# Kernel tuning notes

Measured on AMD Instinct MI355X. Metric: run time of the kernel, lower is better.

## Reference

```python
import jax, jax.numpy as jnp
import numpy as np

N_NODES = 20000
N_EDGES = 320000
NUM_FEAT = 14
DIM = 256


def setup_inputs() -> dict:
    key = jax.random.key(0)
    ks = jax.random.split(key, 12)
    x = jax.random.normal(ks[0], (N_NODES, NUM_FEAT), dtype=jnp.float32)
    edge_index = jax.random.randint(ks[1], (2, N_EDGES), 0, N_NODES, dtype=jnp.int64)
    edge_weight = jax.random.uniform(ks[2], (N_EDGES,), dtype=jnp.float32)

    def lin_w(k, fan_in, fan_out):
        b = 1.0 / np.sqrt(fan_in)
        return jax.random.uniform(k, (fan_in, fan_out), jnp.float32, -b, b)

    params = {
        'W1_rel': lin_w(ks[3], NUM_FEAT, DIM), 'b1_rel': jnp.zeros((DIM,), jnp.float32),
        'W1_root': lin_w(ks[4], NUM_FEAT, DIM),
        'W2_rel': lin_w(ks[5], DIM, DIM), 'b2_rel': jnp.zeros((DIM,), jnp.float32),
        'W2_root': lin_w(ks[6], DIM, DIM),
        'W3_rel': lin_w(ks[7], DIM, DIM), 'b3_rel': jnp.zeros((DIM,), jnp.float32),
        'W3_root': lin_w(ks[8], DIM, DIM),
        'W_lin': lin_w(ks[9], 3 * DIM, DIM), 'b_lin': jnp.zeros((DIM,), jnp.float32),
    }
    return {'x': x, 'edge_index': edge_index, 'edge_weight': edge_weight, **params}


def _graph_conv(x, src, dst, ew, W_rel, b_rel, W_root, n_nodes):
    # message: x_j * w_ij ; aggr='mean' over incoming edges (count, not weight sum)
    msg = x[src] * ew[:, None]                               # [E, F]
    agg = jax.ops.segment_sum(msg, dst, num_segments=n_nodes)  # [N, F]
    cnt = jax.ops.segment_sum(jnp.ones_like(ew), dst, num_segments=n_nodes)
    mean = agg / jnp.maximum(cnt, 1.0)[:, None]
    return mean @ W_rel + b_rel + x @ W_root


def reference(x, edge_index, edge_weight,
              W1_rel, b1_rel, W1_root,
              W2_rel, b2_rel, W2_root,
              W3_rel, b3_rel, W3_root,
              W_lin, b_lin):
    src, dst = edge_index[0], edge_index[1]
    n = x.shape[0]
    # eval mode: dropout is identity
    x1 = jax.nn.relu(_graph_conv(x, src, dst, edge_weight, W1_rel, b1_rel, W1_root, n))
    x2 = jax.nn.relu(_graph_conv(x1, src, dst, edge_weight, W2_rel, b2_rel, W2_root, n))
    x3 = jax.nn.relu(_graph_conv(x2, src, dst, edge_weight, W3_rel, b3_rel, W3_root, n))
    xc = jnp.concatenate([x1, x2, x3], axis=-1)              # [N, 3*DIM]
    return xc @ W_lin + b_lin
```

## Files before the change

### kernel.cpp

```cpp
#include <hip/hip_runtime.h>

#define N_NODES 20000
#define N_EDGES 320000
#define NFEAT 14
#define DIM 256

typedef short bf16x8 __attribute__((ext_vector_type(8)));
typedef float f32x4 __attribute__((ext_vector_type(4)));

__device__ __forceinline__ float b2f(unsigned short u) {
    union { unsigned int u; float f; } v; v.u = ((unsigned int)u) << 16; return v.f;
}
__device__ __forceinline__ unsigned short f2b(float f) {
    union { float f; unsigned int u; } v; v.f = f;
    unsigned int r = v.u + 0x7fffu + ((v.u >> 16) & 1u);
    return (unsigned short)(r >> 16);
}


__global__ __launch_bounds__(256) void k_degree(const int* __restrict__ ei, int* __restrict__ cnt) {
    int e = blockIdx.x * 256 + threadIdx.x;
    if (e < N_EDGES) atomicAdd(&cnt[ei[N_EDGES + e]], 1);
}

__global__ __launch_bounds__(256) void k_alloc(const int* __restrict__ cnt,
                                               int* __restrict__ total,
                                               int* __restrict__ row_ptr,
                                               int* __restrict__ cursor) {
    int i = blockIdx.x * 256 + threadIdx.x;
    int lane = threadIdx.x & 63;
    int deg = (i < N_NODES) ? cnt[i] : 0;
    int s = deg;
    for (int o = 1; o < 64; o <<= 1) { int t = __shfl_up(s, o); if (lane >= o) s += t; }
    int wsum = __shfl(s, 63);
    int base = 0;
    if (lane == 63) base = atomicAdd(total, wsum);
    base = __shfl(base, 63);
    int excl = base + s - deg;
    if (i < N_NODES) { row_ptr[i] = excl; cursor[i] = excl; }
}

__global__ __launch_bounds__(256) void k_fill(const int* __restrict__ ei, const float* __restrict__ ew,
                                              int* __restrict__ cursor,
                                              int* __restrict__ csr_src, float* __restrict__ csr_w) {
    int e = blockIdx.x * 256 + threadIdx.x;
    if (e < N_EDGES) {
        int d = ei[N_EDGES + e];
        int p = atomicAdd(&cursor[d], 1);
        csr_src[p] = ei[e];
        csr_w[p] = ew[e];
    }
}


__global__ __launch_bounds__(256) void k_wstage(
    const float* __restrict__ W2r, const float* __restrict__ W2o,
    const float* __restrict__ W3r, const float* __restrict__ W3o,
    const float* __restrict__ Wl, unsigned short* __restrict__ out) {
    __shared__ unsigned short tb[256][33];
    int part = blockIdx.x >> 3, s = blockIdx.x & 7;
    int tid = threadIdx.x;
    const float* W; int koff = 0;
    switch (part) {
        case 0: W = W2r; break;
        case 1: W = W2o; break;
        case 2: W = W3r; break;
        case 3: W = W3o; break;
        default: W = Wl; koff = (part - 4) * 256; break;
    }
#pragma unroll 4
    for (int j = 0; j < 32; ++j) {
        tb[tid][j] = f2b(W[(size_t)(koff + s * 32 + j) * 256 + tid]);
    }
    __syncthreads();
    unsigned short* dst = out + (size_t)part * 65536 + (size_t)s * 8192;
#pragma unroll 4
    for (int i = 0; i < 32; ++i) {
        int flat = i * 256 + tid;
        dst[flat] = tb[flat >> 5][flat & 31];
    }
}


__global__ __launch_bounds__(256) void k_layer1(
    const float* __restrict__ x, const int* __restrict__ row_ptr, const int* __restrict__ cnt,
    const int* __restrict__ csr_src, const float* __restrict__ csr_w,
    const float* __restrict__ Wrel, const float* __restrict__ brel, const float* __restrict__ Wroot,
    unsigned short* __restrict__ x1b) {
    __shared__ float sWrel[NFEAT][DIM];
    __shared__ float sWroot[NFEAT][DIM];
    __shared__ float sb[DIM];
    int tid = threadIdx.x;
    for (int i = tid; i < NFEAT * DIM; i += 256) {
        (&sWrel[0][0])[i] = Wrel[i];
        (&sWroot[0][0])[i] = Wroot[i];
    }
    if (tid < DIM) sb[tid] = brel[tid];
    __syncthreads();

    int wv = tid >> 6, lane = tid & 63;
    int esub = lane >> 4, k = lane & 15;
    bool kval = (k < NFEAT);

    for (int n8 = 0; n8 < 8; ++n8) {
        int node = blockIdx.x * 32 + n8 * 4 + wv;
        int start = row_ptr[node], deg = cnt[node];
        int end = start + deg;

        float acc = 0.f;
        for (int e0 = start; e0 < end; e0 += 4) {
            int e = e0 + esub;
            if (e < end && kval) {
                int s = csr_src[e];
                acc += x[(size_t)s * NFEAT + k] * csr_w[e];
            }
        }
        acc += __shfl_xor(acc, 16);
        acc += __shfl_xor(acc, 32);
        float macc = acc / fmaxf((float)deg, 1.f);

        float av[NFEAT], xr[NFEAT];
#pragma unroll
        for (int k2 = 0; k2 < NFEAT; ++k2) av[k2] = __shfl(macc, k2);
#pragma unroll
        for (int k2 = 0; k2 < NFEAT; ++k2) xr[k2] = x[(size_t)node * NFEAT + k2];

#pragma unroll
        for (int j = 0; j < 4; ++j) {
            int d = lane + 64 * j;
            float o = sb[d];
#pragma unroll
            for (int k2 = 0; k2 < NFEAT; ++k2)
                o += av[k2] * sWrel[k2][d] + xr[k2] * sWroot[k2][d];
            x1b[(size_t)node * DIM + d] = f2b(fmaxf(o, 0.f));
        }
    }
}


__global__ __launch_bounds__(256) void k_spmm_mean(
    const unsigned short* __restrict__ xin, const int* __restrict__ row_ptr,
    const int* __restrict__ cnt, const int* __restrict__ csr_src,
    const float* __restrict__ csr_w, unsigned short* __restrict__ meanb) {
    int wv = threadIdx.x >> 6, lane = threadIdx.x & 63;
    int node = blockIdx.x * 4 + wv;
    int start = row_ptr[node], deg = cnt[node];
    float a0 = 0.f, a1 = 0.f, a2 = 0.f, a3 = 0.f;
    for (int e = start; e < start + deg; ++e) {
        int s = csr_src[e];
        float w = csr_w[e];
        ushort4 v = *(const ushort4*)(xin + (size_t)s * DIM + lane * 4);
        a0 += b2f(v.x) * w; a1 += b2f(v.y) * w; a2 += b2f(v.z) * w; a3 += b2f(v.w) * w;
    }
    float inv = 1.f / fmaxf((float)deg, 1.f);
    ushort4 o;
    o.x = f2b(a0 * inv); o.y = f2b(a1 * inv); o.z = f2b(a2 * inv); o.w = f2b(a3 * inv);
    *(ushort4*)(meanb + (size_t)node * DIM + lane * 4) = o;
}


__global__ __launch_bounds__(256) void k_gemm_mfma(
    const unsigned short* __restrict__ A0, const unsigned short* __restrict__ A1,
    const unsigned short* __restrict__ A2,
    const unsigned short* __restrict__ B0, const unsigned short* __restrict__ B1,
    const unsigned short* __restrict__ B2,
    int nparts, const float* __restrict__ bias,
    unsigned short* __restrict__ outb, float* __restrict__ outf, int do_relu) {
    __shared__ __align__(16) unsigned short Bs[256][40];
    int t = threadIdx.x;
    int l = t & 63, wv = t >> 6;
    int rowPanel = wv >> 1, colPanel = wv & 1;
    int row0 = blockIdx.x * 32;
    int lr = l & 15, kg = l >> 4;
    int row_a = row0 + rowPanel * 16 + lr;

    f32x4 acc[8];
#pragma unroll
    for (int i = 0; i < 8; i++) acc[i] = (f32x4){0.f, 0.f, 0.f, 0.f};

    for (int p = 0; p < nparts; ++p) {
        const unsigned short* A = (p == 0) ? A0 : (p == 1) ? A1 : A2;
        const unsigned short* B = (p == 0) ? B0 : (p == 1) ? B1 : B2;
        for (int s = 0; s < 8; ++s) {
            const int4* src = (const int4*)(B + (size_t)s * 8192 + (size_t)t * 32);
            int4 v0 = src[0], v1 = src[1], v2 = src[2], v3 = src[3];
            *(int4*)&Bs[t][0]  = v0;
            *(int4*)&Bs[t][8]  = v1;
            *(int4*)&Bs[t][16] = v2;
            *(int4*)&Bs[t][24] = v3;
            __syncthreads();
            bf16x8 a = *(const bf16x8*)(A + (size_t)row_a * DIM + s * 32 + kg * 8);
#pragma unroll
            for (int ct = 0; ct < 8; ++ct) {
                int col = colPanel * 128 + ct * 16 + lr;
                bf16x8 b = *(const bf16x8*)&Bs[col][kg * 8];
                acc[ct] = __builtin_amdgcn_mfma_f32_16x16x32_bf16(a, b, acc[ct], 0, 0, 0);
            }
            __syncthreads();
        }
    }

#pragma unroll
    for (int ct = 0; ct < 8; ++ct) {
        int col = colPanel * 128 + ct * 16 + lr;
        float bv = bias[col];
#pragma unroll
        for (int r = 0; r < 4; ++r) {
            int row = row0 + rowPanel * 16 + kg * 4 + r;
            float v = acc[ct][r] + bv;
            if (do_relu) v = fmaxf(v, 0.f);
            if (outb) outb[(size_t)row * DIM + col] = f2b(v);
            else      outf[(size_t)row * DIM + col] = v;
        }
    }
}


extern "C" void kernel_launch(void* const* d_in, const int* in_sizes, int n_in,
                              void* d_out, int out_size, void* d_ws, size_t ws_size,
                              hipStream_t stream) {
    (void)in_sizes; (void)n_in; (void)out_size; (void)ws_size;
    const float* x       = (const float*)d_in[0];
    const int*   ei      = (const int*)d_in[1];
    const float* ew      = (const float*)d_in[2];
    const float* W1_rel  = (const float*)d_in[3];
    const float* b1      = (const float*)d_in[4];
    const float* W1_root = (const float*)d_in[5];
    const float* W2_rel  = (const float*)d_in[6];
    const float* b2      = (const float*)d_in[7];
    const float* W2_root = (const float*)d_in[8];
    const float* W3_rel  = (const float*)d_in[9];
    const float* b3      = (const float*)d_in[10];
    const float* W3_root = (const float*)d_in[11];
    const float* W_lin   = (const float*)d_in[12];
    const float* b_lin   = (const float*)d_in[13];
    float* out = (float*)d_out;

    char* ws = (char*)d_ws;
    size_t off = 0;
    auto alloc = [&](size_t bytes) -> void* {
        off = (off + 255) & ~(size_t)255;
        void* p = ws + off;
        off += bytes;
        return p;
    };
    int*   cnt     = (int*)alloc((size_t)(N_NODES + 1) * 4);
    int*   row_ptr = (int*)alloc((size_t)N_NODES * 4);
    int*   cursor  = (int*)alloc((size_t)N_NODES * 4);
    int*   csr_src = (int*)alloc((size_t)N_EDGES * 4);
    float* csr_w   = (float*)alloc((size_t)N_EDGES * 4);
    unsigned short* wst   = (unsigned short*)alloc((size_t)7 * 65536 * 2);
    unsigned short* meanb = (unsigned short*)alloc((size_t)N_NODES * DIM * 2);
    unsigned short* x1b   = (unsigned short*)alloc((size_t)N_NODES * DIM * 2);
    unsigned short* x2b   = (unsigned short*)alloc((size_t)N_NODES * DIM * 2);
    unsigned short* x3b   = (unsigned short*)alloc((size_t)N_NODES * DIM * 2);
    int* total = cnt + N_NODES;

    hipMemsetAsync(cnt, 0, (size_t)(N_NODES + 1) * 4, stream);

    int eblocks = (N_EDGES + 255) / 256;
    k_degree<<<eblocks, 256, 0, stream>>>(ei, cnt);
    k_alloc<<<(N_NODES + 255) / 256, 256, 0, stream>>>(cnt, total, row_ptr, cursor);
    k_fill<<<eblocks, 256, 0, stream>>>(ei, ew, cursor, csr_src, csr_w);

    k_wstage<<<56, 256, 0, stream>>>(W2_rel, W2_root, W3_rel, W3_root, W_lin, wst);

    k_layer1<<<N_NODES / 32, 256, 0, stream>>>(x, row_ptr, cnt, csr_src, csr_w,
                                               W1_rel, b1, W1_root, x1b);

    const int ggrid = N_NODES / 32;

    k_spmm_mean<<<N_NODES / 4, 256, 0, stream>>>(x1b, row_ptr, cnt, csr_src, csr_w, meanb);
    k_gemm_mfma<<<ggrid, 256, 0, stream>>>(meanb, x1b, nullptr,
                                           wst, wst + 65536, nullptr,
                                           2, b2, x2b, nullptr, 1);

    k_spmm_mean<<<N_NODES / 4, 256, 0, stream>>>(x2b, row_ptr, cnt, csr_src, csr_w, meanb);
    k_gemm_mfma<<<ggrid, 256, 0, stream>>>(meanb, x2b, nullptr,
                                           wst + 2 * 65536, wst + 3 * 65536, nullptr,
                                           2, b3, x3b, nullptr, 1);

    k_gemm_mfma<<<ggrid, 256, 0, stream>>>(x1b, x2b, x3b,
                                           wst + 4 * 65536, wst + 5 * 65536, wst + 6 * 65536,
                                           3, b_lin, nullptr, out, 0);
}
```

Baseline: 350.9 us.

## Split layer-1 aggregation into a separate kernel and unroll edge gathers by four

Layer-1 neighbour aggregation moves out of the fused dense kernel into its own kernel, which gives each node 16 lanes and writes a padded 16-float mean buffer; the dense kernel then reads that buffer with vector loads. Both the 14-feature aggregation and the bf16 SpMM loop now issue four independent gathers per iteration, raising memory-level parallelism on the irregular reads. The cost is an extra launch and an extra intermediate buffer round-trip, and tail edges are padded with zero-weight duplicate loads.

```diff
diff --git a/kernel.cpp b/kernel.cpp
--- a/kernel.cpp
+++ b/kernel.cpp
@@ -82,11 +82,37 @@
 }
 
 
-__global__ __launch_bounds__(256) void k_layer1(
+__global__ __launch_bounds__(256) void k_agg14(
     const float* __restrict__ x, const int* __restrict__ row_ptr, const int* __restrict__ cnt,
     const int* __restrict__ csr_src, const float* __restrict__ csr_w,
-    const float* __restrict__ Wrel, const float* __restrict__ brel, const float* __restrict__ Wroot,
-    unsigned short* __restrict__ x1b) {
+    float* __restrict__ agg) {
+    int t = blockIdx.x * 256 + threadIdx.x;
+    int node = t >> 4, k = t & 15;
+    int start = row_ptr[node], deg = cnt[node], end = start + deg;
+    bool kv = (k < NFEAT);
+    float acc = 0.f;
+    for (int e0 = start; e0 < end; e0 += 4) {
+        int rem = end - e0;
+        int s0 = csr_src[e0];                    float w0 = csr_w[e0];
+        int s1 = (rem > 1) ? csr_src[e0 + 1] : s0; float w1 = (rem > 1) ? csr_w[e0 + 1] : 0.f;
+        int s2 = (rem > 2) ? csr_src[e0 + 2] : s0; float w2 = (rem > 2) ? csr_w[e0 + 2] : 0.f;
+        int s3 = (rem > 3) ? csr_src[e0 + 3] : s0; float w3 = (rem > 3) ? csr_w[e0 + 3] : 0.f;
+        if (kv) {
+            float x0 = x[(size_t)s0 * NFEAT + k];
+            float x1 = x[(size_t)s1 * NFEAT + k];
+            float x2 = x[(size_t)s2 * NFEAT + k];
+            float x3 = x[(size_t)s3 * NFEAT + k];
+            acc += x0 * w0 + x1 * w1 + x2 * w2 + x3 * w3;
+        }
+    }
+    agg[(size_t)node * 16 + k] = kv ? acc / fmaxf((float)deg, 1.f) : 0.f;
+}
+
+
+__global__ __launch_bounds__(256) void k_l1dense(
+    const float* __restrict__ x, const float* __restrict__ agg,
+    const float* __restrict__ Wrel, const float* __restrict__ brel,
+    const float* __restrict__ Wroot, unsigned short* __restrict__ x1b) {
     __shared__ float sWrel[NFEAT][DIM];
     __shared__ float sWroot[NFEAT][DIM];
     __shared__ float sb[DIM];
@@ -99,31 +125,18 @@
     __syncthreads();
 
     int wv = tid >> 6, lane = tid & 63;
-    int esub = lane >> 4, k = lane & 15;
-    bool kval = (k < NFEAT);
-
     for (int n8 = 0; n8 < 8; ++n8) {
         int node = blockIdx.x * 32 + n8 * 4 + wv;
-        int start = row_ptr[node], deg = cnt[node];
-        int end = start + deg;
-
-        float acc = 0.f;
-        for (int e0 = start; e0 < end; e0 += 4) {
-            int e = e0 + esub;
-            if (e < end && kval) {
-                int s = csr_src[e];
-                acc += x[(size_t)s * NFEAT + k] * csr_w[e];
-            }
-        }
-        acc += __shfl_xor(acc, 16);
-        acc += __shfl_xor(acc, 32);
-        float macc = acc / fmaxf((float)deg, 1.f);
-
         float av[NFEAT], xr[NFEAT];
-#pragma unroll
-        for (int k2 = 0; k2 < NFEAT; ++k2) av[k2] = __shfl(macc, k2);
-#pragma unroll
-        for (int k2 = 0; k2 < NFEAT; ++k2) xr[k2] = x[(size_t)node * NFEAT + k2];
+        const float4* ag4 = (const float4*)(agg + (size_t)node * 16);
+        float4 a0 = ag4[0], a1 = ag4[1], a2 = ag4[2], a3 = ag4[3];
+        av[0]=a0.x; av[1]=a0.y; av[2]=a0.z; av[3]=a0.w;
+        av[4]=a1.x; av[5]=a1.y; av[6]=a1.z; av[7]=a1.w;
+        av[8]=a2.x; av[9]=a2.y; av[10]=a2.z; av[11]=a2.w;
+        av[12]=a3.x; av[13]=a3.y;
+        const float2* xr2 = (const float2*)(x + (size_t)node * NFEAT);
+#pragma unroll
+        for (int k2 = 0; k2 < 7; ++k2) { float2 v = xr2[k2]; xr[2*k2] = v.x; xr[2*k2+1] = v.y; }
 
 #pragma unroll
         for (int j = 0; j < 4; ++j) {
@@ -144,13 +157,22 @@
     const float* __restrict__ csr_w, unsigned short* __restrict__ meanb) {
     int wv = threadIdx.x >> 6, lane = threadIdx.x & 63;
     int node = blockIdx.x * 4 + wv;
-    int start = row_ptr[node], deg = cnt[node];
+    int start = row_ptr[node], deg = cnt[node], end = start + deg;
     float a0 = 0.f, a1 = 0.f, a2 = 0.f, a3 = 0.f;
-    for (int e = start; e < start + deg; ++e) {
-        int s = csr_src[e];
-        float w = csr_w[e];
-        ushort4 v = *(const ushort4*)(xin + (size_t)s * DIM + lane * 4);
-        a0 += b2f(v.x) * w; a1 += b2f(v.y) * w; a2 += b2f(v.z) * w; a3 += b2f(v.w) * w;
+    for (int e0 = start; e0 < end; e0 += 4) {
+        int rem = end - e0;
+        int s0 = csr_src[e0];                    float w0 = csr_w[e0];
+        int s1 = (rem > 1) ? csr_src[e0 + 1] : s0; float w1 = (rem > 1) ? csr_w[e0 + 1] : 0.f;
+        int s2 = (rem > 2) ? csr_src[e0 + 2] : s0; float w2 = (rem > 2) ? csr_w[e0 + 2] : 0.f;
+        int s3 = (rem > 3) ? csr_src[e0 + 3] : s0; float w3 = (rem > 3) ? csr_w[e0 + 3] : 0.f;
+        ushort4 v0 = *(const ushort4*)(xin + (size_t)s0 * DIM + lane * 4);
+        ushort4 v1 = *(const ushort4*)(xin + (size_t)s1 * DIM + lane * 4);
+        ushort4 v2 = *(const ushort4*)(xin + (size_t)s2 * DIM + lane * 4);
+        ushort4 v3 = *(const ushort4*)(xin + (size_t)s3 * DIM + lane * 4);
+        a0 += b2f(v0.x) * w0 + b2f(v1.x) * w1 + b2f(v2.x) * w2 + b2f(v3.x) * w3;
+        a1 += b2f(v0.y) * w0 + b2f(v1.y) * w1 + b2f(v2.y) * w2 + b2f(v3.y) * w3;
+        a2 += b2f(v0.z) * w0 + b2f(v1.z) * w1 + b2f(v2.z) * w2 + b2f(v3.z) * w3;
+        a3 += b2f(v0.w) * w0 + b2f(v1.w) * w1 + b2f(v2.w) * w2 + b2f(v3.w) * w3;
     }
     float inv = 1.f / fmaxf((float)deg, 1.f);
     ushort4 o;
@@ -249,6 +271,7 @@
     int*   cursor  = (int*)alloc((size_t)N_NODES * 4);
     int*   csr_src = (int*)alloc((size_t)N_EDGES * 4);
     float* csr_w   = (float*)alloc((size_t)N_EDGES * 4);
+    float* agg     = (float*)alloc((size_t)N_NODES * 16 * 4);
     unsigned short* wst   = (unsigned short*)alloc((size_t)7 * 65536 * 2);
     unsigned short* meanb = (unsigned short*)alloc((size_t)N_NODES * DIM * 2);
     unsigned short* x1b   = (unsigned short*)alloc((size_t)N_NODES * DIM * 2);
@@ -265,8 +288,8 @@
 
     k_wstage<<<56, 256, 0, stream>>>(W2_rel, W2_root, W3_rel, W3_root, W_lin, wst);
 
-    k_layer1<<<N_NODES / 32, 256, 0, stream>>>(x, row_ptr, cnt, csr_src, csr_w,
-                                               W1_rel, b1, W1_root, x1b);
+    k_agg14<<<N_NODES * 16 / 256, 256, 0, stream>>>(x, row_ptr, cnt, csr_src, csr_w, agg);
+    k_l1dense<<<N_NODES / 32, 256, 0, stream>>>(x, agg, W1_rel, b1, W1_root, x1b);
 
     const int ggrid = N_NODES / 32;
 
```

New measurement: 287.8 us. 18.0% less time.
